# Kernel optimization log

Measured on AMD Instinct MI355X. Metric: run time of the kernel, lower is better.

## Reference

```python
import jax, jax.numpy as jnp
import numpy as np

NUM_QUANTIZERS = 8
CODEBOOK_SIZE = 1024
DIM = 64
B, N = 8, 8192


def setup_inputs() -> dict:
    key = jax.random.key(0)
    kx, kc = jax.random.split(key)
    x = jax.random.normal(kx, (B, N, DIM), dtype=jnp.float32)
    # one codebook per quantizer stage (shared_codebook=False)
    codebooks = jax.random.normal(kc, (NUM_QUANTIZERS, CODEBOOK_SIZE, DIM), dtype=jnp.float32)
    return {"x": x, "codebooks": codebooks}


def reference(x, codebooks):
    """Residual VQ: sequential nearest-codebook lookup with residual subtraction.

    x:         [b, n, d]
    codebooks: [Q, K, d]
    returns quantized_out: [b, n, d]
    """

    def step(carry, cb):
        residual, qout = carry                       # [b,n,d], [b,n,d]
        # squared euclidean distances, [b,n,K]
        r_sq = jnp.sum(residual * residual, axis=-1, keepdims=True)
        c_sq = jnp.sum(cb * cb, axis=-1)             # [K]
        dots = jnp.einsum('bnd,kd->bnk', residual, cb)
        dist = r_sq - 2.0 * dots + c_sq              # [b,n,K]
        idx = jnp.argmin(dist, axis=-1)              # [b,n]
        quant = cb[idx]                              # [b,n,d] gather
        # straight-through estimator (VectorQuantize forward)
        quant_st = residual + jax.lax.stop_gradient(quant - residual)
        new_residual = residual - jax.lax.stop_gradient(quant)
        return (new_residual, qout + quant_st), idx

    init = (x, jnp.zeros_like(x))
    (residual, quantized_out), all_indices = jax.lax.scan(step, init, codebooks)
    return quantized_out
```

## Files before the change

kernel.cpp:

```cpp
#include <hip/hip_runtime.h>

#define NQ 8
#define KCODES 1024
#define D 64
#define CHUNK 64
#define NCHUNK 16
#define TPB 256
#define TOKPB 64
#define BIAS 96.0f

using short8 = __attribute__((ext_vector_type(8))) short;
using f32x4  = __attribute__((ext_vector_type(4))) float;

#define GLOBAL_AS __attribute__((address_space(1)))
#define LDS_AS    __attribute__((address_space(3)))

static __device__ __forceinline__ unsigned bf16_rne_bits(float f) {
    unsigned u = __float_as_uint(f);
    return (u + 0x7fffu + ((u >> 16) & 1u)) >> 16;
}
static __device__ __forceinline__ unsigned umn(unsigned a, unsigned b) { return a < b ? a : b; }
static __device__ __forceinline__ unsigned umx(unsigned a, unsigned b) { return a > b ? a : b; }
static __device__ __forceinline__ unsigned umed3(unsigned a, unsigned b, unsigned c) {
    return umx(umn(a, b), umn(umx(a, b), c));
}

__global__ __launch_bounds__(256) void prep_cb(const float* __restrict__ cb,
                                               int4* __restrict__ ws_cb) {
    int id = blockIdx.x * 256 + threadIdx.x;
    int n_rel = id & 63;
    int plane = (id >> 6) & 15;
    int ch    = (id >> 10) & 15;
    int q     = id >> 14;
    int g = plane & 3, kt = (plane >> 2) & 1, term = plane >> 3;
    int n = ch * CHUNK + n_rel;
    const float* src = cb + ((size_t)(q * KCODES + n)) * D + kt * 32 + g * 8;
    union { short s[8]; int4 v; } u;
    #pragma unroll
    for (int j = 0; j < 8; ++j) {
        float f = -src[j];
        unsigned hb = bf16_rne_bits(f);
        if (term == 0) {
            u.s[j] = (short)hb;
        } else {
            float lo = f - __uint_as_float(hb << 16);
            u.s[j] = (short)bf16_rne_bits(lo);
        }
    }
    ws_cb[id] = u.v;
}

__global__ __launch_bounds__(256) void prep_csq(const float* __restrict__ cb,
                                                float* __restrict__ ws_csq,
                                                float* __restrict__ ws_csqh) {
    int id = blockIdx.x * 256 + threadIdx.x;
    const float* c = cb + (size_t)id * D;
    float s0 = 0.f, s1 = 0.f, s2 = 0.f, s3 = 0.f;
    #pragma unroll
    for (int j = 0; j < 16; ++j) {
        s0 = fmaf(c[4*j+0], c[4*j+0], s0);
        s1 = fmaf(c[4*j+1], c[4*j+1], s1);
        s2 = fmaf(c[4*j+2], c[4*j+2], s2);
        s3 = fmaf(c[4*j+3], c[4*j+3], s3);
    }
    float cs = (s0 + s1) + (s2 + s3);
    ws_csq[id]  = cs;
    ws_csqh[id] = 0.5f * cs + BIAS;
}

__global__ __launch_bounds__(TPB, 4) void rvq_mfma(
    const float* __restrict__ x,
    const float* __restrict__ cb,
    const int4* __restrict__ ws_cb,
    const float* __restrict__ ws_csq,
    float* __restrict__ out)
{
    __shared__ __align__(16) int4  lds_stage[1024];
    __shared__ __align__(16) float lds_resid[TOKPB * 68];
    __shared__ float    lds_csqh[CHUNK];
    __shared__ unsigned lds_cand[2][TOKPB * 3];
    __shared__ int      lds_pick[TOKPB];

    const int tid   = threadIdx.x;
    const int lane  = tid & 63;
    const int wave  = tid >> 6;
    const int group = wave >> 1;
    const int half  = wave & 1;
    const int g     = lane >> 4;
    const int c     = lane & 15;
    const int tok0  = blockIdx.x * TOKPB;

    {
        const int t = tid >> 2, part = tid & 3;
        const float4* xp = (const float4*)(x + (size_t)(tok0 + t) * D + part * 16);
        float4* rr = (float4*)(lds_resid + t * 68 + part * 16);
        #pragma unroll
        for (int k2 = 0; k2 < 4; ++k2) rr[k2] = xp[k2];
    }

    const char* bp = (const char*)lds_stage + (c << 4) + (g << 10) + half * 512;

    for (int q = 0; q < NQ; ++q) {
        __syncthreads();

        short8 ah0[2], ah1[2], al0[2], al1[2];
        #pragma unroll
        for (int s = 0; s < 2; ++s) {
            const float* rr = lds_resid + (group * 32 + s * 16 + c) * 68;
            float4 f0 = *(const float4*)(rr + 8 * g);
            float4 f1 = *(const float4*)(rr + 8 * g + 4);
            float4 f2 = *(const float4*)(rr + 32 + 8 * g);
            float4 f3 = *(const float4*)(rr + 36 + 8 * g);
            const float* v0 = (const float*)&f0;
            const float* v1 = (const float*)&f1;
            const float* v2 = (const float*)&f2;
            const float* v3 = (const float*)&f3;
            #pragma unroll
            for (int j = 0; j < 4; ++j) {
                float a = v0[j], b = v1[j], e = v2[j], f = v3[j];
                unsigned ha = bf16_rne_bits(a);
                unsigned hb = bf16_rne_bits(b);
                unsigned he = bf16_rne_bits(e);
                unsigned hf = bf16_rne_bits(f);
                ah0[s][j]   = (short)ha;  ah0[s][4+j] = (short)hb;
                ah1[s][j]   = (short)he;  ah1[s][4+j] = (short)hf;
                al0[s][j]   = (short)bf16_rne_bits(a - __uint_as_float(ha << 16));
                al0[s][4+j] = (short)bf16_rne_bits(b - __uint_as_float(hb << 16));
                al1[s][j]   = (short)bf16_rne_bits(e - __uint_as_float(he << 16));
                al1[s][4+j] = (short)bf16_rne_bits(f - __uint_as_float(hf << 16));
            }
        }

        unsigned T1[2][4], T2[2][4], T3[2][4];
        #pragma unroll
        for (int s = 0; s < 2; ++s)
            #pragma unroll
            for (int r = 0; r < 4; ++r) { T1[s][r] = 0xFFFFFFFFu; T2[s][r] = 0xFFFFFFFFu; T3[s][r] = 0xFFFFFFFFu; }

        for (int ch = 0; ch < NCHUNK; ++ch) {
            __syncthreads();
            {
                const int4* src = ws_cb + (size_t)(q * NCHUNK + ch) * 1024 + tid;
                LDS_AS char* ldst = (LDS_AS char*)lds_stage + tid * 16;
                #pragma unroll
                for (int t = 0; t < 4; ++t) {
                    __builtin_amdgcn_global_load_lds(
                        (const GLOBAL_AS unsigned int*)(src + t * 256),
                        (LDS_AS unsigned int*)(ldst + t * 4096), 16, 0, 0);
                }
                if (tid < CHUNK) {
                    __builtin_amdgcn_global_load_lds(
                        (const GLOBAL_AS unsigned int*)(ws_csq + 8192 + q * KCODES + ch * CHUNK + tid),
                        (LDS_AS unsigned int*)(&lds_csqh[tid]), 4, 0, 0);
                }
            }
            __syncthreads();

            #pragma unroll
            for (int i = 0; i < 2; ++i) {
                short8 bh0 = *(const short8*)(bp + i * 256);
                short8 bh1 = *(const short8*)(bp + 4096  + i * 256);
                short8 bl0 = *(const short8*)(bp + 8192  + i * 256);
                short8 bl1 = *(const short8*)(bp + 12288 + i * 256);
                const float sd = lds_csqh[(half * 2 + i) * 16 + c];
                const unsigned codev = (unsigned)(ch * CHUNK + (half * 2 + i) * 16 + c);
                #pragma unroll
                for (int s = 0; s < 2; ++s) {
                    f32x4 acc = {sd, sd, sd, sd};
                    acc = __builtin_amdgcn_mfma_f32_16x16x32_bf16(ah0[s], bh0, acc, 0, 0, 0);
                    acc = __builtin_amdgcn_mfma_f32_16x16x32_bf16(ah1[s], bh1, acc, 0, 0, 0);
                    acc = __builtin_amdgcn_mfma_f32_16x16x32_bf16(al0[s], bh0, acc, 0, 0, 0);
                    acc = __builtin_amdgcn_mfma_f32_16x16x32_bf16(ah0[s], bl0, acc, 0, 0, 0);
                    acc = __builtin_amdgcn_mfma_f32_16x16x32_bf16(al1[s], bh1, acc, 0, 0, 0);
                    acc = __builtin_amdgcn_mfma_f32_16x16x32_bf16(ah1[s], bl1, acc, 0, 0, 0);
                    #pragma unroll
                    for (int r = 0; r < 4; ++r) {
                        unsigned p = (__float_as_uint(acc[r]) & 0xFFFFFC00u) | codev;
                        unsigned n2 = umn(T2[s][r], umx(T1[s][r], p));
                        unsigned n3 = umn(T3[s][r], umx(T2[s][r], p));
                        T1[s][r] = umn(T1[s][r], p);
                        T2[s][r] = n2;
                        T3[s][r] = n3;
                    }
                }
            }
        }

        #pragma unroll
        for (int st = 1; st <= 8; st <<= 1) {
            #pragma unroll
            for (int s = 0; s < 2; ++s) {
                #pragma unroll
                for (int r = 0; r < 4; ++r) {
                    unsigned o1 = (unsigned)__shfl_xor((int)T1[s][r], st);
                    unsigned o2 = (unsigned)__shfl_xor((int)T2[s][r], st);
                    unsigned o3 = (unsigned)__shfl_xor((int)T3[s][r], st);
                    unsigned x1 = umn(T1[s][r], o1), y1 = umx(T1[s][r], o1);
                    unsigned x2 = umn(T2[s][r], o2), y2 = umx(T2[s][r], o2);
                    unsigned x3 = umn(T3[s][r], o3);
                    T1[s][r] = x1;
                    T3[s][r] = umed3(y1, x2, umn(y2, x3));
                    T2[s][r] = umn(y1, x2);
                }
            }
        }

        if (c == 0) {
            #pragma unroll
            for (int s = 0; s < 2; ++s)
                #pragma unroll
                for (int r = 0; r < 4; ++r) {
                    const int idx = (group * 32 + s * 16 + g * 4 + r) * 3;
                    lds_cand[half][idx + 0] = T1[s][r];
                    lds_cand[half][idx + 1] = T2[s][r];
                    lds_cand[half][idx + 2] = T3[s][r];
                }
        }
        __syncthreads();

        {
            const int t4  = lane >> 2;
            const int sel = lane & 3;
            const int row = group * 32 + half * 16 + t4;
            unsigned a1 = lds_cand[0][row * 3 + 0];
            unsigned a2 = lds_cand[0][row * 3 + 1];
            unsigned a3 = lds_cand[0][row * 3 + 2];
            unsigned b1 = lds_cand[1][row * 3 + 0];
            unsigned b2 = lds_cand[1][row * 3 + 1];
            unsigned b3 = lds_cand[1][row * 3 + 2];
            unsigned x1 = umn(a1, b1), y1 = umx(a1, b1);
            unsigned x2 = umn(a2, b2), y2 = umx(a2, b2);
            unsigned x3 = umn(a3, b3);
            unsigned m1 = x1;
            unsigned m2 = umn(y1, x2);
            unsigned m3 = umed3(y1, x2, umn(y2, x3));
            const unsigned psel = (sel == 0) ? m1 : ((sel == 1) ? m2 : m3);
            const int cd = (int)(psel & 1023u);

            const float4* rrv = (const float4*)(lds_resid + row * 68);
            const float4* cpv = (const float4*)(cb + ((size_t)(q * KCODES + cd)) * D);
            float ax = 0.f, ay = 0.f, az = 0.f, aw = 0.f;
            #pragma unroll
            for (int j = 0; j < 16; ++j) {
                float4 rv = rrv[j];
                float4 cv = cpv[j];
                ax = fmaf(rv.x, cv.x, ax);
                ay = fmaf(rv.y, cv.y, ay);
                az = fmaf(rv.z, cv.z, az);
                aw = fmaf(rv.w, cv.w, aw);
            }
            float dot = (ax + ay) + (az + aw);
            float dd = fmaf(dot, -2.0f, ws_csq[q * KCODES + cd]);

            const int base = lane & ~3;
            float d0 = __shfl(dd, base);
            float d1 = __shfl(dd, base + 1);
            float d2 = __shfl(dd, base + 2);
            int cc0 = (int)(m1 & 1023u);
            int cc1 = (int)(m2 & 1023u);
            int cc2 = (int)(m3 & 1023u);
            float db = d0; int pick = cc0;
            if (d1 < db || (d1 == db && cc1 < pick)) { db = d1; pick = cc1; }
            if (d2 < db || (d2 == db && cc2 < pick)) { db = d2; pick = cc2; }
            if (sel == 0) lds_pick[row] = pick;
        }
        __syncthreads();

        {
            const int t = tid >> 2, part = tid & 3;
            const int ifin = lds_pick[t];
            const float4* cp = (const float4*)(cb + ((size_t)(q * KCODES + ifin)) * D + part * 16);
            float4* rr = (float4*)(lds_resid + t * 68 + part * 16);
            #pragma unroll
            for (int k2 = 0; k2 < 4; ++k2) {
                float4 rv = rr[k2], cv = cp[k2];
                rv.x -= cv.x; rv.y -= cv.y; rv.z -= cv.z; rv.w -= cv.w;
                rr[k2] = rv;
            }
        }
    }

    __syncthreads();
    {
        const int t = tid >> 2, part = tid & 3;
        const float4* xp = (const float4*)(x + (size_t)(tok0 + t) * D + part * 16);
        const float4* rr = (const float4*)(lds_resid + t * 68 + part * 16);
        float4* op = (float4*)(out + (size_t)(tok0 + t) * D + part * 16);
        #pragma unroll
        for (int k2 = 0; k2 < 4; ++k2) {
            float4 xv = xp[k2], rv = rr[k2];
            float4 o;
            o.x = xv.x - rv.x; o.y = xv.y - rv.y;
            o.z = xv.z - rv.z; o.w = xv.w - rv.w;
            op[k2] = o;
        }
    }
}

extern "C" void kernel_launch(void* const* d_in, const int* in_sizes, int n_in,
                              void* d_out, int out_size, void* d_ws, size_t ws_size,
                              hipStream_t stream) {
    const float* x  = (const float*)d_in[0];
    const float* cb = (const float*)d_in[1];
    float* out = (float*)d_out;

    int4*  ws_cb   = (int4*)d_ws;
    float* ws_csq  = (float*)((char*)d_ws + (size_t)2 * 1024 * 1024);
    float* ws_csqh = ws_csq + 8192;

    prep_cb <<<512, 256, 0, stream>>>(cb, ws_cb);
    prep_csq<<< 32, 256, 0, stream>>>(cb, ws_csq, ws_csqh);

    const int n_tokens = in_sizes[0] / D;
    const int grid = n_tokens / TOKPB;
    rvq_mfma<<<grid, TPB, 0, stream>>>(x, cb, ws_cb, ws_csq, out);
}
```

Before: 347.6 us.

## Double-buffer codebook chunks in LDS with prefetch and use v_med3 for top-3

After: 337.9 us. 2.8% less time.

```diff
diff --git a/kernel.cpp b/kernel.cpp
--- a/kernel.cpp
+++ b/kernel.cpp
@@ -5,6 +5,8 @@
 #define D 64
 #define CHUNK 64
 #define NCHUNK 16
+#define CH32 32
+#define NGI (NQ * 32)
 #define TPB 256
 #define TOKPB 64
 #define BIAS 96.0f
@@ -22,7 +24,9 @@
 static __device__ __forceinline__ unsigned umn(unsigned a, unsigned b) { return a < b ? a : b; }
 static __device__ __forceinline__ unsigned umx(unsigned a, unsigned b) { return a > b ? a : b; }
 static __device__ __forceinline__ unsigned umed3(unsigned a, unsigned b, unsigned c) {
-    return umx(umn(a, b), umn(umx(a, b), c));
+    unsigned d;
+    asm("v_med3_u32 %0, %1, %2, %3" : "=v"(d) : "v"(a), "v"(b), "v"(c));
+    return d;
 }
 
 __global__ __launch_bounds__(256) void prep_cb(const float* __restrict__ cb,
@@ -68,6 +72,54 @@
     ws_csqh[id] = 0.5f * cs + BIAS;
 }
 
+#define CHUNK_BODY(BUF, GI)                                                               \
+  {                                                                                       \
+    __syncthreads();                                                                      \
+    if ((GI) + 1 < NGI) {                                                                 \
+      const int gin = (GI) + 1;                                                           \
+      const int qn = gin >> 5, chn = gin & 31;                                            \
+      const int4* srcn = ws_cb + (((qn * 16 + (chn >> 1)) << 10) + ((chn & 1) << 5));     \
+      _Pragma("unroll")                                                                   \
+      for (int t = 0; t < 2; ++t) {                                                       \
+        const int id = t * 256 + tid;                                                     \
+        __builtin_amdgcn_global_load_lds(                                                 \
+            (const GLOBAL_AS unsigned int*)(srcn + ((id >> 5) << 6) + (id & 31)),         \
+            (LDS_AS unsigned int*)((LDS_AS char*)&lds_stage[(BUF) ^ 1][0] + id * 16),     \
+            16, 0, 0);                                                                    \
+      }                                                                                   \
+      if (tid < CH32) {                                                                   \
+        __builtin_amdgcn_global_load_lds(                                                 \
+            (const GLOBAL_AS unsigned int*)(ws_csqh + qn * KCODES + chn * CH32 + tid),    \
+            (LDS_AS unsigned int*)(&lds_csqh[(BUF) ^ 1][tid]), 4, 0, 0);                  \
+      }                                                                                   \
+    }                                                                                     \
+    const char* bb = (const char*)&lds_stage[(BUF)][0] + bB;                              \
+    short8 bh0 = *(const short8*)(bb);                                                    \
+    short8 bh1 = *(const short8*)(bb + 2048);                                             \
+    short8 bl0 = *(const short8*)(bb + 4096);                                             \
+    short8 bl1 = *(const short8*)(bb + 6144);                                             \
+    const float sd = lds_csqh[(BUF)][half * 16 + c];                                      \
+    const unsigned codev = (unsigned)((((GI) & 31) << 5) + (half << 4) + c);              \
+    _Pragma("unroll")                                                                     \
+    for (int s = 0; s < 2; ++s) {                                                         \
+      f32x4 acc = {sd, sd, sd, sd};                                                       \
+      acc = __builtin_amdgcn_mfma_f32_16x16x32_bf16(ah0[s], bh0, acc, 0, 0, 0);           \
+      acc = __builtin_amdgcn_mfma_f32_16x16x32_bf16(ah1[s], bh1, acc, 0, 0, 0);           \
+      acc = __builtin_amdgcn_mfma_f32_16x16x32_bf16(al0[s], bh0, acc, 0, 0, 0);           \
+      acc = __builtin_amdgcn_mfma_f32_16x16x32_bf16(ah0[s], bl0, acc, 0, 0, 0);           \
+      acc = __builtin_amdgcn_mfma_f32_16x16x32_bf16(al1[s], bh1, acc, 0, 0, 0);           \
+      acc = __builtin_amdgcn_mfma_f32_16x16x32_bf16(ah1[s], bl1, acc, 0, 0, 0);           \
+      _Pragma("unroll")                                                                   \
+      for (int r = 0; r < 4; ++r) {                                                       \
+        const unsigned p = (__float_as_uint(acc[r]) & 0xFFFFFC00u) | codev;               \
+        const unsigned t1o = T1[s][r], t2o = T2[s][r];                                    \
+        T1[s][r] = umn(t1o, p);                  \
+        T2[s][r] = umed3(t1o, t2o, p);          \
+        T3[s][r] = umed3(t2o, T3[s][r], p);      \
+      }                                                                                   \
+    }                                                                                     \
+  }
+
 __global__ __launch_bounds__(TPB, 4) void rvq_mfma(
     const float* __restrict__ x,
     const float* __restrict__ cb,
@@ -75,9 +127,9 @@
     const float* __restrict__ ws_csq,
     float* __restrict__ out)
 {
-    __shared__ __align__(16) int4  lds_stage[1024];
+    __shared__ __align__(16) int4  lds_stage[2][512];
     __shared__ __align__(16) float lds_resid[TOKPB * 68];
-    __shared__ float    lds_csqh[CHUNK];
+    __shared__ float    lds_csqh[2][CH32];
     __shared__ unsigned lds_cand[2][TOKPB * 3];
     __shared__ int      lds_pick[TOKPB];
 
@@ -89,6 +141,22 @@
     const int g     = lane >> 4;
     const int c     = lane & 15;
     const int tok0  = blockIdx.x * TOKPB;
+    const float* ws_csqh = ws_csq + 8192;
+
+    {
+        #pragma unroll
+        for (int t = 0; t < 2; ++t) {
+            const int id = t * 256 + tid;
+            __builtin_amdgcn_global_load_lds(
+                (const GLOBAL_AS unsigned int*)(ws_cb + ((id >> 5) << 6) + (id & 31)),
+                (LDS_AS unsigned int*)((LDS_AS char*)&lds_stage[0][0] + id * 16), 16, 0, 0);
+        }
+        if (tid < CH32) {
+            __builtin_amdgcn_global_load_lds(
+                (const GLOBAL_AS unsigned int*)(ws_csqh + tid),
+                (LDS_AS unsigned int*)(&lds_csqh[0][tid]), 4, 0, 0);
+        }
+    }
 
     {
         const int t = tid >> 2, part = tid & 3;
@@ -98,7 +166,7 @@
         for (int k2 = 0; k2 < 4; ++k2) rr[k2] = xp[k2];
     }
 
-    const char* bp = (const char*)lds_stage + (c << 4) + (g << 10) + half * 512;
+    const int bB = (g << 9) + ((half * 16 + c) << 4);
 
     for (int q = 0; q < NQ; ++q) {
         __syncthreads();
@@ -137,53 +205,10 @@
             #pragma unroll
             for (int r = 0; r < 4; ++r) { T1[s][r] = 0xFFFFFFFFu; T2[s][r] = 0xFFFFFFFFu; T3[s][r] = 0xFFFFFFFFu; }
 
-        for (int ch = 0; ch < NCHUNK; ++ch) {
-            __syncthreads();
-            {
-                const int4* src = ws_cb + (size_t)(q * NCHUNK + ch) * 1024 + tid;
-                LDS_AS char* ldst = (LDS_AS char*)lds_stage + tid * 16;
-                #pragma unroll
-                for (int t = 0; t < 4; ++t) {
-                    __builtin_amdgcn_global_load_lds(
-                        (const GLOBAL_AS unsigned int*)(src + t * 256),
-                        (LDS_AS unsigned int*)(ldst + t * 4096), 16, 0, 0);
-                }
-                if (tid < CHUNK) {
-                    __builtin_amdgcn_global_load_lds(
-                        (const GLOBAL_AS unsigned int*)(ws_csq + 8192 + q * KCODES + ch * CHUNK + tid),
-                        (LDS_AS unsigned int*)(&lds_csqh[tid]), 4, 0, 0);
-                }
-            }
-            __syncthreads();
-
-            #pragma unroll
-            for (int i = 0; i < 2; ++i) {
-                short8 bh0 = *(const short8*)(bp + i * 256);
-                short8 bh1 = *(const short8*)(bp + 4096  + i * 256);
-                short8 bl0 = *(const short8*)(bp + 8192  + i * 256);
-                short8 bl1 = *(const short8*)(bp + 12288 + i * 256);
-                const float sd = lds_csqh[(half * 2 + i) * 16 + c];
-                const unsigned codev = (unsigned)(ch * CHUNK + (half * 2 + i) * 16 + c);
-                #pragma unroll
-                for (int s = 0; s < 2; ++s) {
-                    f32x4 acc = {sd, sd, sd, sd};
-                    acc = __builtin_amdgcn_mfma_f32_16x16x32_bf16(ah0[s], bh0, acc, 0, 0, 0);
-                    acc = __builtin_amdgcn_mfma_f32_16x16x32_bf16(ah1[s], bh1, acc, 0, 0, 0);
-                    acc = __builtin_amdgcn_mfma_f32_16x16x32_bf16(al0[s], bh0, acc, 0, 0, 0);
-                    acc = __builtin_amdgcn_mfma_f32_16x16x32_bf16(ah0[s], bl0, acc, 0, 0, 0);
-                    acc = __builtin_amdgcn_mfma_f32_16x16x32_bf16(al1[s], bh1, acc, 0, 0, 0);
-                    acc = __builtin_amdgcn_mfma_f32_16x16x32_bf16(ah1[s], bl1, acc, 0, 0, 0);
-                    #pragma unroll
-                    for (int r = 0; r < 4; ++r) {
-                        unsigned p = (__float_as_uint(acc[r]) & 0xFFFFFC00u) | codev;
-                        unsigned n2 = umn(T2[s][r], umx(T1[s][r], p));
-                        unsigned n3 = umn(T3[s][r], umx(T2[s][r], p));
-                        T1[s][r] = umn(T1[s][r], p);
-                        T2[s][r] = n2;
-                        T3[s][r] = n3;
-                    }
-                }
-            }
+        for (int cp = 0; cp < 16; ++cp) {
+            const int gi0 = (q << 5) + (cp << 1);
+            CHUNK_BODY(0, gi0);
+            CHUNK_BODY(1, gi0 + 1);
         }
 
         #pragma unroll
```

## Load codebook fragments directly from global into registers with prefetch, drop LDS staging

Applied to the files above, without the earlier changes.

After: 346.0 us. No clear change (-0.5%).

```diff
diff --git a/kernel.cpp b/kernel.cpp
--- a/kernel.cpp
+++ b/kernel.cpp
@@ -4,7 +4,6 @@
 #define KCODES 1024
 #define D 64
 #define CHUNK 64
-#define NCHUNK 16
 #define TPB 256
 #define TOKPB 64
 #define BIAS 96.0f
@@ -12,9 +11,6 @@
 using short8 = __attribute__((ext_vector_type(8))) short;
 using f32x4  = __attribute__((ext_vector_type(4))) float;
 
-#define GLOBAL_AS __attribute__((address_space(1)))
-#define LDS_AS    __attribute__((address_space(3)))
-
 static __device__ __forceinline__ unsigned bf16_rne_bits(float f) {
     unsigned u = __float_as_uint(f);
     return (u + 0x7fffu + ((u >> 16) & 1u)) >> 16;
@@ -22,7 +18,9 @@
 static __device__ __forceinline__ unsigned umn(unsigned a, unsigned b) { return a < b ? a : b; }
 static __device__ __forceinline__ unsigned umx(unsigned a, unsigned b) { return a > b ? a : b; }
 static __device__ __forceinline__ unsigned umed3(unsigned a, unsigned b, unsigned c) {
-    return umx(umn(a, b), umn(umx(a, b), c));
+    unsigned d;
+    asm("v_med3_u32 %0, %1, %2, %3" : "=v"(d) : "v"(a), "v"(b), "v"(c));
+    return d;
 }
 
 __global__ __launch_bounds__(256) void prep_cb(const float* __restrict__ cb,
@@ -75,9 +73,8 @@
     const float* __restrict__ ws_csq,
     float* __restrict__ out)
 {
-    __shared__ __align__(16) int4  lds_stage[1024];
     __shared__ __align__(16) float lds_resid[TOKPB * 68];
-    __shared__ float    lds_csqh[CHUNK];
+    __shared__ __align__(16) float lds_csqh_q[KCODES];
     __shared__ unsigned lds_cand[2][TOKPB * 3];
     __shared__ int      lds_pick[TOKPB];
 
@@ -89,6 +86,7 @@
     const int g     = lane >> 4;
     const int c     = lane & 15;
     const int tok0  = blockIdx.x * TOKPB;
+    const float* ws_csqh = ws_csq + 8192;
 
     {
         const int t = tid >> 2, part = tid & 3;
@@ -98,9 +96,14 @@
         for (int k2 = 0; k2 < 4; ++k2) rr[k2] = xp[k2];
     }
 
-    const char* bp = (const char*)lds_stage + (c << 4) + (g << 10) + half * 512;
+    const int lid = (g << 6) + (half << 4) + c;
+    const int sdo = (half << 4) + c;
 
     for (int q = 0; q < NQ; ++q) {
+        {
+            const float4 v = *(const float4*)(ws_csqh + (q << 10) + (tid << 2));
+            *(float4*)(lds_csqh_q + (tid << 2)) = v;
+        }
         __syncthreads();
 
         short8 ah0[2], ah1[2], al0[2], al1[2];
@@ -137,51 +140,41 @@
             #pragma unroll
             for (int r = 0; r < 4; ++r) { T1[s][r] = 0xFFFFFFFFu; T2[s][r] = 0xFFFFFFFFu; T3[s][r] = 0xFFFFFFFFu; }
 
-        for (int ch = 0; ch < NCHUNK; ++ch) {
-            __syncthreads();
-            {
-                const int4* src = ws_cb + (size_t)(q * NCHUNK + ch) * 1024 + tid;
-                LDS_AS char* ldst = (LDS_AS char*)lds_stage + tid * 16;
+        const int4* fpq = ws_cb + ((size_t)q << 14) + lid;
+        short8 nb0 = *(const short8*)(fpq);
+        short8 nb1 = *(const short8*)(fpq + 256);
+        short8 nb2 = *(const short8*)(fpq + 512);
+        short8 nb3 = *(const short8*)(fpq + 768);
+        #pragma unroll 1
+        for (int ch = 0; ch < 32; ++ch) {
+            const short8 bh0 = nb0, bh1 = nb1, bl0 = nb2, bl1 = nb3;
+            if (ch < 31) {
+                const int chn = ch + 1;
+                const int4* fpn = fpq + ((chn >> 1) << 10) + ((chn & 1) << 5);
+                nb0 = *(const short8*)(fpn);
+                nb1 = *(const short8*)(fpn + 256);
+                nb2 = *(const short8*)(fpn + 512);
+                nb3 = *(const short8*)(fpn + 768);
+            }
+            const int cv = (ch << 5) + sdo;
+            const float sd = lds_csqh_q[cv];
+            const unsigned codev = (unsigned)cv;
+            #pragma unroll
+            for (int s = 0; s < 2; ++s) {
+                f32x4 acc = {sd, sd, sd, sd};
+                acc = __builtin_amdgcn_mfma_f32_16x16x32_bf16(ah0[s], bh0, acc, 0, 0, 0);
+                acc = __builtin_amdgcn_mfma_f32_16x16x32_bf16(ah1[s], bh1, acc, 0, 0, 0);
+                acc = __builtin_amdgcn_mfma_f32_16x16x32_bf16(al0[s], bh0, acc, 0, 0, 0);
+                acc = __builtin_amdgcn_mfma_f32_16x16x32_bf16(ah0[s], bl0, acc, 0, 0, 0);
+                acc = __builtin_amdgcn_mfma_f32_16x16x32_bf16(al1[s], bh1, acc, 0, 0, 0);
+                acc = __builtin_amdgcn_mfma_f32_16x16x32_bf16(ah1[s], bl1, acc, 0, 0, 0);
                 #pragma unroll
-                for (int t = 0; t < 4; ++t) {
-                    __builtin_amdgcn_global_load_lds(
-                        (const GLOBAL_AS unsigned int*)(src + t * 256),
-                        (LDS_AS unsigned int*)(ldst + t * 4096), 16, 0, 0);
-                }
-                if (tid < CHUNK) {
-                    __builtin_amdgcn_global_load_lds(
-                        (const GLOBAL_AS unsigned int*)(ws_csq + 8192 + q * KCODES + ch * CHUNK + tid),
-                        (LDS_AS unsigned int*)(&lds_csqh[tid]), 4, 0, 0);
-                }
-            }
-            __syncthreads();
-
-            #pragma unroll
-            for (int i = 0; i < 2; ++i) {
-                short8 bh0 = *(const short8*)(bp + i * 256);
-                short8 bh1 = *(const short8*)(bp + 4096  + i * 256);
-                short8 bl0 = *(const short8*)(bp + 8192  + i * 256);
-                short8 bl1 = *(const short8*)(bp + 12288 + i * 256);
-                const float sd = lds_csqh[(half * 2 + i) * 16 + c];
-                const unsigned codev = (unsigned)(ch * CHUNK + (half * 2 + i) * 16 + c);
-                #pragma unroll
-                for (int s = 0; s < 2; ++s) {
-                    f32x4 acc = {sd, sd, sd, sd};
-                    acc = __builtin_amdgcn_mfma_f32_16x16x32_bf16(ah0[s], bh0, acc, 0, 0, 0);
-                    acc = __builtin_amdgcn_mfma_f32_16x16x32_bf16(ah1[s], bh1, acc, 0, 0, 0);
-                    acc = __builtin_amdgcn_mfma_f32_16x16x32_bf16(al0[s], bh0, acc, 0, 0, 0);
-                    acc = __builtin_amdgcn_mfma_f32_16x16x32_bf16(ah0[s], bl0, acc, 0, 0, 0);
-                    acc = __builtin_amdgcn_mfma_f32_16x16x32_bf16(al1[s], bh1, acc, 0, 0, 0);
-                    acc = __builtin_amdgcn_mfma_f32_16x16x32_bf16(ah1[s], bl1, acc, 0, 0, 0);
-                    #pragma unroll
-                    for (int r = 0; r < 4; ++r) {
-                        unsigned p = (__float_as_uint(acc[r]) & 0xFFFFFC00u) | codev;
-                        unsigned n2 = umn(T2[s][r], umx(T1[s][r], p));
-                        unsigned n3 = umn(T3[s][r], umx(T2[s][r], p));
-                        T1[s][r] = umn(T1[s][r], p);
-                        T2[s][r] = n2;
-                        T3[s][r] = n3;
-                    }
+                for (int r = 0; r < 4; ++r) {
+                    const unsigned p = (__float_as_uint(acc[r]) & 0xFFFFFC00u) | codev;
+                    const unsigned t1o = T1[s][r], t2o = T2[s][r];
+                    T1[s][r] = umn(t1o, p);
+                    T2[s][r] = umed3(t1o, t2o, p);
+                    T3[s][r] = umed3(t2o, T3[s][r], p);
                 }
             }
         }
```
